# Optimization experiments

Hardware: AMD Instinct MI355X
Metric: run time of the kernel (lower is better)

## Reference

```python
import jax, jax.numpy as jnp
import numpy as np

B, T, NH, EX, VOCAB, NLAYER = 8, 510, 12, 768, 256, 6
NBLK = 2 * NLAYER - 1          # 11 blocks, all with out=ex
NE = T + 2                     # CustomEmb output dim = n_embd = 512
HD = EX // NH
EXIT_SCALE = 1.0 / float(np.sqrt(4 * NBLK))  # torch init divides 'exit' params by sqrt(#exit params)


def _ln(x, s, b):
    m = jnp.mean(x, axis=-1, keepdims=True)
    v = jnp.mean((x - m) ** 2, axis=-1, keepdims=True)
    return (x - m) * jax.lax.rsqrt(v + 1e-5) * s + b


def setup_inputs() -> dict:
    key = jax.random.key(0)
    ks = iter(jax.random.split(key, 40))
    def n(shape, scale=0.02):
        return jax.random.normal(next(ks), shape, jnp.float32) * scale
    inp = {}
    inp['idx'] = jax.random.randint(next(ks), (B, T), 0, 2)
    inp['lin_w'] = n((NE, EX)); inp['lin_b'] = n((EX,))
    # stacked per-block params (leading dim NBLK), torch Linear math y = x @ W + b with W stored (in,out)
    inp['ln1_s'] = jnp.ones((NBLK, EX), jnp.float32); inp['ln1_b'] = jnp.zeros((NBLK, EX), jnp.float32)
    inp['qw'] = n((NBLK, EX, EX)); inp['qb'] = n((NBLK, EX))
    inp['kw'] = n((NBLK, EX, EX)); inp['kb'] = n((NBLK, EX))
    inp['vw'] = n((NBLK, EX, EX)); inp['vb'] = n((NBLK, EX))
    inp['ew'] = n((NBLK, EX, EX)) * EXIT_SCALE; inp['eb'] = n((NBLK, EX)) * EXIT_SCALE
    inp['ln2_s'] = jnp.ones((NBLK, EX), jnp.float32); inp['ln2_b'] = jnp.zeros((NBLK, EX), jnp.float32)
    inp['m1w'] = n((NBLK, EX, 4 * EX)); inp['m1b'] = n((NBLK, 4 * EX))
    inp['m2w'] = n((NBLK, 4 * EX, EX)) * EXIT_SCALE; inp['m2b'] = n((NBLK, EX)) * EXIT_SCALE
    inp['lnf_s'] = jnp.ones((EX,), jnp.float32); inp['lnf_b'] = jnp.zeros((EX,), jnp.float32)
    inp['head_w'] = n((EX * T, VOCAB)); inp['head_b'] = n((VOCAB,))
    return inp


def reference(idx, lin_w, lin_b, ln1_s, ln1_b, qw, qb, kw, kb, vw, vb, ew, eb,
              ln2_s, ln2_b, m1w, m1b, m2w, m2b, lnf_s, lnf_b, head_w, head_b):
    # CustomEmb: one-hot of binary token + identity positional encoding -> [B,T,T+2]
    e0 = (idx == 0).astype(jnp.float32)
    e1 = (idx == 1).astype(jnp.float32)
    pos = jnp.broadcast_to(jnp.eye(T, dtype=jnp.float32), (B, T, T))
    x = jnp.concatenate([e0[:, :, None], e1[:, :, None], pos], axis=2)
    x = jax.nn.relu(x @ lin_w + lin_b)                       # [B,T,EX]
    mask = jnp.tril(jnp.ones((T, T), bool))
    inv_sqrt_d = 1.0 / float(np.sqrt(HD))

    def block(x, p):
        l1s, l1b, Qw, Qb, Kw, Kb, Vw, Vb, Ew, Eb, l2s, l2b, M1w, M1b, M2w, M2b = p
        h = _ln(x, l1s, l1b)
        q = (h @ Qw + Qb).reshape(B, T, NH, HD)
        k = (h @ Kw + Kb).reshape(B, T, NH, HD)
        v = (h @ Vw + Vb).reshape(B, T, NH, HD)
        att = jnp.einsum('bqhd,bkhd->bhqk', q, k) * inv_sqrt_d
        att = jnp.where(mask, att, -jnp.inf)
        probs = jax.nn.softmax(att, axis=-1)
        y = jnp.einsum('bhqk,bkhd->bqhd', probs, v).reshape(B, T, EX)
        x = x + y @ Ew + Eb
        h2 = _ln(x, l2s, l2b)
        x = x + jax.nn.relu(h2 @ M1w + M1b) @ M2w + M2b      # MLP depth=2: initial+relu+exit
        return x, None

    x, _ = jax.lax.scan(block, x, (ln1_s, ln1_b, qw, qb, kw, kb, vw, vb,
                                   ew, eb, ln2_s, ln2_b, m1w, m1b, m2w, m2b))
    x = _ln(x, lnf_s, lnf_b)
    return x.reshape(B, -1) @ head_w + head_b                # [B, VOCAB]
```

## Files before the change

kernel.cpp:

```cpp
#include <hip/hip_runtime.h>
#include <hip/hip_bf16.h>
#include <math.h>

constexpr int cB = 8, cT = 510, cNH = 12, cEX = 768, cVOC = 256, cNBLK = 11, cHD = 64;
constexpr int cMB = 512;
constexpr int cMP = 4096;
constexpr int cQKV = 3 * cEX;

typedef __attribute__((ext_vector_type(8))) short bf16x8;
typedef __attribute__((ext_vector_type(4))) float f32x4;
using bf16 = __hip_bfloat16;

__device__ inline void gload16(const void* g, void* l) {
    __builtin_amdgcn_global_load_lds((const __attribute__((address_space(1))) unsigned int*)g,
                                     (__attribute__((address_space(3))) unsigned int*)l, 16, 0, 0);
}
__device__ inline short f2bs(float f) {
    bf16 b = __float2bfloat16(f);
    return *reinterpret_cast<short*>(&b);
}

__global__ __launch_bounds__(256) void embed_kernel(
    const int* __restrict__ idx, const float* __restrict__ lin_w,
    const float* __restrict__ lin_b, float* __restrict__ x)
{
    int row = blockIdx.x;
    int b = row >> 9, t = row & 511;
    float* xr = x + (size_t)row * cEX;
    if (t >= cT) {
        for (int j = threadIdx.x; j < cEX; j += 256) xr[j] = 0.0f;
        return;
    }
    int tok = idx[b * cT + t] & 1;
    const float* wt = lin_w + (size_t)tok * cEX;
    const float* wp = lin_w + (size_t)(2 + t) * cEX;
    for (int j = threadIdx.x; j < cEX; j += 256) {
        float val = wt[j] + wp[j] + lin_b[j];
        xr[j] = fmaxf(val, 0.0f);
    }
}

template<typename OUT>
__global__ __launch_bounds__(256) void ln_wave(
    const float* __restrict__ in, const float* __restrict__ s,
    const float* __restrict__ bsh, OUT* __restrict__ out)
{
    const int wid = threadIdx.x >> 6, lane = threadIdx.x & 63;
    const int row = blockIdx.x * 4 + wid;
    const float* xr = in + (size_t)row * cEX;
    float4 v[3];
    float sum = 0.f, sq = 0.f;
#pragma unroll
    for (int p = 0; p < 3; ++p) {
        v[p] = *(const float4*)&xr[p * 256 + lane * 4];
        sum += v[p].x + v[p].y + v[p].z + v[p].w;
        sq  += v[p].x * v[p].x + v[p].y * v[p].y + v[p].z * v[p].z + v[p].w * v[p].w;
    }
#pragma unroll
    for (int off = 1; off < 64; off <<= 1) {
        sum += __shfl_xor(sum, off, 64);
        sq  += __shfl_xor(sq, off, 64);
    }
    float mean = sum * (1.0f / cEX);
    float var = sq * (1.0f / cEX) - mean * mean;
    float rstd = rsqrtf(var + 1e-5f);
    OUT* outr = out + (size_t)row * cEX;
#pragma unroll
    for (int p = 0; p < 3; ++p) {
        int c = p * 256 + lane * 4;
        float4 sv = *(const float4*)&s[c];
        float4 bv = *(const float4*)&bsh[c];
        float o0 = (v[p].x - mean) * rstd * sv.x + bv.x;
        float o1 = (v[p].y - mean) * rstd * sv.y + bv.y;
        float o2 = (v[p].z - mean) * rstd * sv.z + bv.z;
        float o3 = (v[p].w - mean) * rstd * sv.w + bv.w;
        if constexpr (sizeof(OUT) == 2) {
            short4 pk;
            pk.x = f2bs(o0); pk.y = f2bs(o1); pk.z = f2bs(o2); pk.w = f2bs(o3);
            *(short4*)&outr[c] = pk;
        } else {
            *(float4*)&outr[c] = make_float4(o0, o1, o2, o3);
        }
    }
}

__global__ __launch_bounds__(256) void transpose_w(
    const float* __restrict__ W, bf16* __restrict__ WT,
    int K, int N, size_t w_stride, size_t wt_stride, int wt_row_off)
{
    __shared__ float t[32][33];
    const float* Wb = W + (size_t)blockIdx.z * w_stride;
    bf16* WTb = WT + (size_t)blockIdx.z * wt_stride;
    int n0 = blockIdx.x * 32, k0 = blockIdx.y * 32;
    int c = threadIdx.x & 31, ty = threadIdx.x >> 5;
#pragma unroll
    for (int it = 0; it < 4; ++it) {
        int r = ty + it * 8;
        t[r][c] = Wb[(size_t)(k0 + r) * N + n0 + c];
    }
    __syncthreads();
#pragma unroll
    for (int it = 0; it < 4; ++it) {
        int a = ty + it * 8;
        WTb[(size_t)(wt_row_off + n0 + a) * K + k0 + c] = __float2bfloat16(t[c][a]);
    }
}

__global__ __launch_bounds__(256) void concat_bias(
    const float* __restrict__ qb, const float* __restrict__ kb,
    const float* __restrict__ vb, float* __restrict__ qkvb)
{
    int i = blockIdx.x * 256 + threadIdx.x;
    if (i >= cNBLK * cQKV) return;
    int blk = i / cQKV, c = i - blk * cQKV;
    const float* src; int cc = c;
    if (c < cEX)            { src = qb; }
    else if (c < 2 * cEX)   { src = kb; cc = c - cEX; }
    else                    { src = vb; cc = c - 2 * cEX; }
    qkvb[i] = src[(size_t)blk * cEX + cc];
}

template<int FM, int FN, bool RELU, bool RESID, bool OUTBF16, bool VT>
__global__ __launch_bounds__(256) void gemm_db(
    const short* __restrict__ A, const short* __restrict__ BT,
    const float* __restrict__ bias, const float* __restrict__ resid,
    void* __restrict__ Cout, short* __restrict__ vTr, int K, int N)
{
    constexpr int BM = FM * 32, BN = FN * 32;
    constexpr int TS = (BM + BN) * 64;
    constexpr int CA = BM / 32, CB = BN / 32;
    constexpr int LPT = CA + CB;
    __shared__ short lds[2 * TS];
    const int tid = threadIdx.x;
    const int lane = tid & 63, wid = tid >> 6;
    const int wm = wid >> 1, wn = wid & 1;
    const int bm = blockIdx.y * BM, bn = blockIdx.x * BN;
    const int li = lane & 15, gk = lane >> 4;

    f32x4 acc[FM][FN];
#pragma unroll
    for (int i = 0; i < FM; ++i)
#pragma unroll
        for (int j = 0; j < FN; ++j)
            acc[i][j] = f32x4{0.f, 0.f, 0.f, 0.f};

    auto stage = [&](int kt, int buf) {
        short* la = &lds[buf * TS];
        short* lb = la + BM * 64;
#pragma unroll
        for (int i = 0; i < CA; ++i) {
            int s = i * 256 + tid;
            int r = s >> 3, c = s & 7;
            gload16(A + (size_t)(bm + r) * K + kt * 64 + (c ^ (r & 7)) * 8,
                    (char*)la + (size_t)(i * 256 + wid * 64) * 16);
        }
#pragma unroll
        for (int i = 0; i < CB; ++i) {
            int s = i * 256 + tid;
            int r = s >> 3, c = s & 7;
            gload16(BT + (size_t)(bn + r) * K + kt * 64 + (c ^ (r & 7)) * 8,
                    (char*)lb + (size_t)(i * 256 + wid * 64) * 16);
        }
    };

    const int nkt = K >> 6;
    stage(0, 0);
    stage(1, 1);

    for (int t = 0; t < nkt; ++t) {
        if (t + 1 < nkt) {
            if constexpr (LPT == 8) asm volatile("s_waitcnt vmcnt(8)" ::: "memory");
            else                    asm volatile("s_waitcnt vmcnt(6)" ::: "memory");
        } else {
            asm volatile("s_waitcnt vmcnt(0)" ::: "memory");
        }
        __builtin_amdgcn_s_barrier();

        const short* la = &lds[(t & 1) * TS];
        const short* lb = la + BM * 64;
        bf16x8 af[FM][2], bf_[FN][2];
#pragma unroll
        for (int mi = 0; mi < FM; ++mi) {
            int row = wm * FM * 16 + mi * 16 + li;
#pragma unroll
            for (int ks = 0; ks < 2; ++ks)
                af[mi][ks] = *(const bf16x8*)&la[row * 64 + ((ks * 4 + gk) ^ (row & 7)) * 8];
        }
#pragma unroll
        for (int ni = 0; ni < FN; ++ni) {
            int row = wn * FN * 16 + ni * 16 + li;
#pragma unroll
            for (int ks = 0; ks < 2; ++ks)
                bf_[ni][ks] = *(const bf16x8*)&lb[row * 64 + ((ks * 4 + gk) ^ (row & 7)) * 8];
        }
        __builtin_amdgcn_s_setprio(1);
#pragma unroll
        for (int ks = 0; ks < 2; ++ks)
#pragma unroll
            for (int mi = 0; mi < FM; ++mi)
#pragma unroll
                for (int ni = 0; ni < FN; ++ni)
                    acc[mi][ni] = __builtin_amdgcn_mfma_f32_16x16x32_bf16(
                        af[mi][ks], bf_[ni][ks], acc[mi][ni], 0, 0, 0);
        __builtin_amdgcn_s_setprio(0);

        asm volatile("" ::: "memory");
        __builtin_amdgcn_s_barrier();
        if (t + 2 < nkt) stage(t + 2, t & 1);
    }

#pragma unroll
    for (int mi = 0; mi < FM; ++mi) {
#pragma unroll
        for (int ni = 0; ni < FN; ++ni) {
            int col = bn + wn * FN * 16 + ni * 16 + li;
            float bv = bias[col];
            int row0 = bm + wm * FM * 16 + mi * 16 + gk * 4;
            if (VT && col >= 2 * cEX) {
                short4 pk;
                pk.x = f2bs(acc[mi][ni][0] + bv);
                pk.y = f2bs(acc[mi][ni][1] + bv);
                pk.z = f2bs(acc[mi][ni][2] + bv);
                pk.w = f2bs(acc[mi][ni][3] + bv);
                *(short4*)&vTr[(size_t)(col - 2 * cEX) * cMP + row0] = pk;
            } else {
#pragma unroll
                for (int j = 0; j < 4; ++j) {
                    int row = row0 + j;
                    float v = acc[mi][ni][j] + bv;
                    if (RELU) v = fmaxf(v, 0.0f);
                    if (RESID) v += resid[(size_t)row * N + col];
                    if (OUTBF16)
                        ((bf16*)Cout)[(size_t)row * N + col] = __float2bfloat16(v);
                    else
                        ((float*)Cout)[(size_t)row * N + col] = v;
                }
            }
        }
    }
}

__global__ __launch_bounds__(256) void attn_mfma(
    const short* __restrict__ qkv, const short* __restrict__ vT, bf16* __restrict__ y)
{
    const int qt = blockIdx.x, h = blockIdx.y, b = blockIdx.z;
    __shared__ short Ks[32 * 64];
    __shared__ short Vs[64 * 32];
    __shared__ short Ss[4][16][40];
    const int tid = threadIdx.x;
    const int lane = tid & 63, wid = tid >> 6;
    const int li = lane & 15, gk = lane >> 4;

    const size_t rowb = (size_t)b * cMB;
    int qr = qt * 64 + wid * 16 + li;
    int qrc = qr < cT ? qr : cT - 1;
    const short* qrow = qkv + (rowb + qrc) * cQKV + h * cHD;
    bf16x8 qf0 = *(const bf16x8*)(qrow + gk * 8);
    bf16x8 qf1 = *(const bf16x8*)(qrow + 32 + gk * 8);

    f32x4 o[4];
    float mrow[4], lrow[4];
#pragma unroll
    for (int dt = 0; dt < 4; ++dt) o[dt] = f32x4{0.f, 0.f, 0.f, 0.f};
#pragma unroll
    for (int j = 0; j < 4; ++j) { mrow[j] = -3e38f; lrow[j] = 0.f; }

    const int kkey = tid >> 3, kclog = (tid & 7) ^ (kkey & 7);
    const int vd = tid >> 2,  vclog = (tid & 3) ^ (vd & 3);
    const int qloc = qt * 64 + wid * 16 + gk * 4;

    const int nkt = 2 * qt + 2;
    for (int kt = 0; kt < nkt; ++kt) {
        gload16(qkv + (rowb + kt * 32 + kkey) * cQKV + cEX + h * cHD + kclog * 8,
                (char*)Ks + wid * 1024);
        gload16(vT + (size_t)(h * cHD + vd) * cMP + rowb + kt * 32 + vclog * 8,
                (char*)Vs + wid * 1024);
        __syncthreads();

        f32x4 s0 = f32x4{0.f, 0.f, 0.f, 0.f}, s1 = f32x4{0.f, 0.f, 0.f, 0.f};
        {
            int key0 = li, key1 = 16 + li;
            bf16x8 k00 = *(const bf16x8*)&Ks[key0 * 64 + ((0 + gk) ^ (key0 & 7)) * 8];
            bf16x8 k01 = *(const bf16x8*)&Ks[key0 * 64 + ((4 + gk) ^ (key0 & 7)) * 8];
            bf16x8 k10 = *(const bf16x8*)&Ks[key1 * 64 + ((0 + gk) ^ (key1 & 7)) * 8];
            bf16x8 k11 = *(const bf16x8*)&Ks[key1 * 64 + ((4 + gk) ^ (key1 & 7)) * 8];
            s0 = __builtin_amdgcn_mfma_f32_16x16x32_bf16(qf0, k00, s0, 0, 0, 0);
            s0 = __builtin_amdgcn_mfma_f32_16x16x32_bf16(qf1, k01, s0, 0, 0, 0);
            s1 = __builtin_amdgcn_mfma_f32_16x16x32_bf16(qf0, k10, s1, 0, 0, 0);
            s1 = __builtin_amdgcn_mfma_f32_16x16x32_bf16(qf1, k11, s1, 0, 0, 0);
        }

        float sc0[4], sc1[4];
#pragma unroll
        for (int j = 0; j < 4; ++j) {
            int q = qloc + j;
            int key0 = kt * 32 + li, key1 = key0 + 16;
            sc0[j] = (key0 <= q) ? s0[j] * 0.125f : -3e38f;
            sc1[j] = (key1 <= q) ? s1[j] * 0.125f : -3e38f;
        }
        float p0[4], p1[4];
#pragma unroll
        for (int j = 0; j < 4; ++j) {
            float tm = fmaxf(sc0[j], sc1[j]);
            tm = fmaxf(tm, __shfl_xor(tm, 1, 16));
            tm = fmaxf(tm, __shfl_xor(tm, 2, 16));
            tm = fmaxf(tm, __shfl_xor(tm, 4, 16));
            tm = fmaxf(tm, __shfl_xor(tm, 8, 16));
            float mnew = fmaxf(mrow[j], tm);
            p0[j] = __expf(sc0[j] - mnew);
            p1[j] = __expf(sc1[j] - mnew);
            float ps = p0[j] + p1[j];
            ps += __shfl_xor(ps, 1, 16);
            ps += __shfl_xor(ps, 2, 16);
            ps += __shfl_xor(ps, 4, 16);
            ps += __shfl_xor(ps, 8, 16);
            float scale = __expf(mrow[j] - mnew);
            lrow[j] = lrow[j] * scale + ps;
            mrow[j] = mnew;
#pragma unroll
            for (int dt = 0; dt < 4; ++dt) o[dt][j] *= scale;
        }
#pragma unroll
        for (int j = 0; j < 4; ++j) {
            Ss[wid][gk * 4 + j][li]      = f2bs(p0[j]);
            Ss[wid][gk * 4 + j][16 + li] = f2bs(p1[j]);
        }
        bf16x8 pa = *(const bf16x8*)&Ss[wid][li][gk * 8];
#pragma unroll
        for (int dt = 0; dt < 4; ++dt) {
            int d = dt * 16 + li;
            bf16x8 vf = *(const bf16x8*)&Vs[d * 32 + (gk ^ (d & 3)) * 8];
            o[dt] = __builtin_amdgcn_mfma_f32_16x16x32_bf16(pa, vf, o[dt], 0, 0, 0);
        }
        __syncthreads();
    }

#pragma unroll
    for (int j = 0; j < 4; ++j) {
        int q = qloc + j;
        if (q >= cT) continue;
        float inv = 1.0f / lrow[j];
        bf16* yr = y + (rowb + q) * cEX + h * cHD;
#pragma unroll
        for (int dt = 0; dt < 4; ++dt)
            yr[dt * 16 + li] = __float2bfloat16(o[dt][j] * inv);
    }
}

__global__ __launch_bounds__(256) void head_part_kernel(
    const float* __restrict__ xf, const float* __restrict__ hw, float* __restrict__ part)
{
    __shared__ float xs[8][1536];
    const int tid = threadIdx.x;
    const int k0 = blockIdx.x * 1536;
    for (int i = tid; i < 8 * 1536; i += 256) {
        int bb = i / 1536, kk = i - bb * 1536;
        xs[bb][kk] = xf[(size_t)bb * (cMB * cEX) + k0 + kk];
    }
    __syncthreads();
    float acc[8] = {};
    const float* wp = hw + (size_t)k0 * cVOC + tid;
    for (int kk = 0; kk < 1536; ++kk) {
        float w = wp[(size_t)kk * cVOC];
#pragma unroll
        for (int bb = 0; bb < 8; ++bb) acc[bb] += xs[bb][kk] * w;
    }
#pragma unroll
    for (int bb = 0; bb < 8; ++bb)
        part[((size_t)blockIdx.x * 8 + bb) * cVOC + tid] = acc[bb];
}

__global__ __launch_bounds__(256) void head_reduce_kernel(
    const float* __restrict__ part, const float* __restrict__ hb, float* __restrict__ out)
{
    int i = blockIdx.x * 256 + threadIdx.x;
    int bb = i >> 8, vv = i & 255;
    float acc = hb[vv];
    for (int c = 0; c < 255; ++c) acc += part[((size_t)c * 8 + bb) * 256 + vv];
    out[i] = acc;
}

extern "C" void kernel_launch(void* const* d_in, const int* in_sizes, int n_in,
                              void* d_out, int out_size, void* d_ws, size_t ws_size,
                              hipStream_t stream) {
    (void)in_sizes; (void)n_in; (void)out_size; (void)ws_size;
    const int*   idx    = (const int*)d_in[0];
    const float* lin_w  = (const float*)d_in[1];
    const float* lin_b  = (const float*)d_in[2];
    const float* ln1_s  = (const float*)d_in[3];
    const float* ln1_b  = (const float*)d_in[4];
    const float* qw     = (const float*)d_in[5];
    const float* qbias  = (const float*)d_in[6];
    const float* kw     = (const float*)d_in[7];
    const float* kbias  = (const float*)d_in[8];
    const float* vw     = (const float*)d_in[9];
    const float* vbias  = (const float*)d_in[10];
    const float* ew     = (const float*)d_in[11];
    const float* ebias  = (const float*)d_in[12];
    const float* ln2_s  = (const float*)d_in[13];
    const float* ln2_b  = (const float*)d_in[14];
    const float* m1w    = (const float*)d_in[15];
    const float* m1b    = (const float*)d_in[16];
    const float* m2w    = (const float*)d_in[17];
    const float* m2b    = (const float*)d_in[18];
    const float* lnf_s  = (const float*)d_in[19];
    const float* lnf_b  = (const float*)d_in[20];
    const float* head_w = (const float*)d_in[21];
    const float* head_b = (const float*)d_in[22];
    float* out = (float*)d_out;

    const size_t act = (size_t)cMP * cEX;
    float* x    = (float*)d_ws;
    float* xf   = x + act;
    float* part = xf + act;
    float* qkvb = part + 255 * 8 * 256;
    short* qkv  = (short*)(qkvb + cNBLK * cQKV);
    short* vTr  = qkv + (size_t)cMP * cQKV;
    short* h    = vTr + (size_t)cEX * cMP;
    short* h2   = h + act;
    short* y    = h2 + act;
    short* u    = y + act;
    short* wqkvT = u + (size_t)cMP * 4 * cEX;
    short* weT   = wqkvT + (size_t)cNBLK * cQKV * cEX;
    short* wm1T  = weT + (size_t)cNBLK * cEX * cEX;
    short* wm2T  = wm1T + (size_t)cNBLK * cEX * 4 * cEX;

    transpose_w<<<dim3(24, 24, cNBLK), 256, 0, stream>>>(qw, (bf16*)wqkvT, cEX, cEX,
        (size_t)cEX * cEX, (size_t)cQKV * cEX, 0);
    transpose_w<<<dim3(24, 24, cNBLK), 256, 0, stream>>>(kw, (bf16*)wqkvT, cEX, cEX,
        (size_t)cEX * cEX, (size_t)cQKV * cEX, cEX);
    transpose_w<<<dim3(24, 24, cNBLK), 256, 0, stream>>>(vw, (bf16*)wqkvT, cEX, cEX,
        (size_t)cEX * cEX, (size_t)cQKV * cEX, 2 * cEX);
    transpose_w<<<dim3(24, 24, cNBLK), 256, 0, stream>>>(ew, (bf16*)weT, cEX, cEX,
        (size_t)cEX * cEX, (size_t)cEX * cEX, 0);
    transpose_w<<<dim3(96, 24, cNBLK), 256, 0, stream>>>(m1w, (bf16*)wm1T, cEX, 4 * cEX,
        (size_t)cEX * 4 * cEX, (size_t)cEX * 4 * cEX, 0);
    transpose_w<<<dim3(24, 96, cNBLK), 256, 0, stream>>>(m2w, (bf16*)wm2T, 4 * cEX, cEX,
        (size_t)cEX * 4 * cEX, (size_t)cEX * 4 * cEX, 0);
    concat_bias<<<(cNBLK * cQKV + 255) / 256, 256, 0, stream>>>(qbias, kbias, vbias, qkvb);

    embed_kernel<<<cMP, 256, 0, stream>>>(idx, lin_w, lin_b, x);

    for (int blk = 0; blk < cNBLK; ++blk) {
        size_t bo = (size_t)blk * cEX;
        ln_wave<bf16><<<cMP / 4, 256, 0, stream>>>(x, ln1_s + bo, ln1_b + bo, (bf16*)h);
        gemm_db<4, 4, false, false, true, true><<<dim3(cQKV / 128, cMP / 128), 256, 0, stream>>>(
            h, wqkvT + (size_t)blk * cQKV * cEX, qkvb + (size_t)blk * cQKV, nullptr,
            qkv, vTr, cEX, cQKV);
        attn_mfma<<<dim3(8, cNH, cB), 256, 0, stream>>>(qkv, vTr, (bf16*)y);
        gemm_db<2, 4, false, true, false, false><<<dim3(cEX / 128, cMP / 64), 256, 0, stream>>>(
            y, weT + (size_t)blk * cEX * cEX, ebias + bo, x, x, nullptr, cEX, cEX);
        ln_wave<bf16><<<cMP / 4, 256, 0, stream>>>(x, ln2_s + bo, ln2_b + bo, (bf16*)h2);
        gemm_db<4, 4, true, false, true, false><<<dim3(4 * cEX / 128, cMP / 128), 256, 0, stream>>>(
            h2, wm1T + (size_t)blk * cEX * 4 * cEX, m1b + (size_t)blk * 4 * cEX, nullptr,
            u, nullptr, cEX, 4 * cEX);
        gemm_db<2, 4, false, true, false, false><<<dim3(cEX / 128, cMP / 64), 256, 0, stream>>>(
            u, wm2T + (size_t)blk * cEX * 4 * cEX, m2b + bo, x, x, nullptr, 4 * cEX, cEX);
    }
    ln_wave<float><<<cMP / 4, 256, 0, stream>>>(x, lnf_s, lnf_b, xf);
    head_part_kernel<<<255, 256, 0, stream>>>(xf, head_w, part);
    head_reduce_kernel<<<8, 256, 0, stream>>>(part, head_b, out);
}
```

Baseline: 1.889 ms.

## Split GEMM k-step to overlap staging with MFMA; use 64-key attention tiles

In the GEMM main loop, the second half of each 64-wide K tile is now read from LDS before the barrier. The next stage's global-to-LDS load is then issued before the second batch of MFMAs, so the loads overlap with compute. In attention, each iteration now processes 64 keys instead of 32. This halves the number of loop trips, barriers and softmax reductions, at the cost of more LDS and registers and possibly lower occupancy. Causal masking is unchanged, but the diagonal tile now does a full 64-key block of wasted work.

```diff
diff --git a/kernel.cpp b/kernel.cpp
--- a/kernel.cpp
+++ b/kernel.cpp
@@ -178,35 +178,49 @@
 
         const short* la = &lds[(t & 1) * TS];
         const short* lb = la + BM * 64;
-        bf16x8 af[FM][2], bf_[FN][2];
+
+        bf16x8 af0[FM], bf0[FN];
 #pragma unroll
         for (int mi = 0; mi < FM; ++mi) {
             int row = wm * FM * 16 + mi * 16 + li;
-#pragma unroll
-            for (int ks = 0; ks < 2; ++ks)
-                af[mi][ks] = *(const bf16x8*)&la[row * 64 + ((ks * 4 + gk) ^ (row & 7)) * 8];
+            af0[mi] = *(const bf16x8*)&la[row * 64 + (gk ^ (row & 7)) * 8];
         }
 #pragma unroll
         for (int ni = 0; ni < FN; ++ni) {
             int row = wn * FN * 16 + ni * 16 + li;
-#pragma unroll
-            for (int ks = 0; ks < 2; ++ks)
-                bf_[ni][ks] = *(const bf16x8*)&lb[row * 64 + ((ks * 4 + gk) ^ (row & 7)) * 8];
+            bf0[ni] = *(const bf16x8*)&lb[row * 64 + (gk ^ (row & 7)) * 8];
         }
         __builtin_amdgcn_s_setprio(1);
 #pragma unroll
-        for (int ks = 0; ks < 2; ++ks)
-#pragma unroll
-            for (int mi = 0; mi < FM; ++mi)
-#pragma unroll
-                for (int ni = 0; ni < FN; ++ni)
-                    acc[mi][ni] = __builtin_amdgcn_mfma_f32_16x16x32_bf16(
-                        af[mi][ks], bf_[ni][ks], acc[mi][ni], 0, 0, 0);
+        for (int mi = 0; mi < FM; ++mi)
+#pragma unroll
+            for (int ni = 0; ni < FN; ++ni)
+                acc[mi][ni] = __builtin_amdgcn_mfma_f32_16x16x32_bf16(
+                    af0[mi], bf0[ni], acc[mi][ni], 0, 0, 0);
         __builtin_amdgcn_s_setprio(0);
 
-        asm volatile("" ::: "memory");
+        bf16x8 af1[FM], bf1[FN];
+#pragma unroll
+        for (int mi = 0; mi < FM; ++mi) {
+            int row = wm * FM * 16 + mi * 16 + li;
+            af1[mi] = *(const bf16x8*)&la[row * 64 + ((4 + gk) ^ (row & 7)) * 8];
+        }
+#pragma unroll
+        for (int ni = 0; ni < FN; ++ni) {
+            int row = wn * FN * 16 + ni * 16 + li;
+            bf1[ni] = *(const bf16x8*)&lb[row * 64 + ((4 + gk) ^ (row & 7)) * 8];
+        }
+        asm volatile("s_waitcnt lgkmcnt(0)" ::: "memory");
         __builtin_amdgcn_s_barrier();
         if (t + 2 < nkt) stage(t + 2, t & 1);
+        __builtin_amdgcn_s_setprio(1);
+#pragma unroll
+        for (int mi = 0; mi < FM; ++mi)
+#pragma unroll
+            for (int ni = 0; ni < FN; ++ni)
+                acc[mi][ni] = __builtin_amdgcn_mfma_f32_16x16x32_bf16(
+                    af1[mi], bf1[ni], acc[mi][ni], 0, 0, 0);
+        __builtin_amdgcn_s_setprio(0);
     }
 
 #pragma unroll
@@ -244,9 +258,9 @@
     const short* __restrict__ qkv, const short* __restrict__ vT, bf16* __restrict__ y)
 {
     const int qt = blockIdx.x, h = blockIdx.y, b = blockIdx.z;
-    __shared__ short Ks[32 * 64];
-    __shared__ short Vs[64 * 32];
-    __shared__ short Ss[4][16][40];
+    __shared__ short Ks[64 * 64];
+    __shared__ short Vs[64 * 64];
+    __shared__ short Ss[4][16][72];
     const int tid = threadIdx.x;
     const int lane = tid & 63, wid = tid >> 6;
     const int li = lane & 15, gk = lane >> 4;
@@ -265,51 +279,56 @@
 #pragma unroll
     for (int j = 0; j < 4; ++j) { mrow[j] = -3e38f; lrow[j] = 0.f; }
 
-    const int kkey = tid >> 3, kclog = (tid & 7) ^ (kkey & 7);
-    const int vd = tid >> 2,  vclog = (tid & 3) ^ (vd & 3);
     const int qloc = qt * 64 + wid * 16 + gk * 4;
 
-    const int nkt = 2 * qt + 2;
+    const int nkt = qt + 1;
     for (int kt = 0; kt < nkt; ++kt) {
-        gload16(qkv + (rowb + kt * 32 + kkey) * cQKV + cEX + h * cHD + kclog * 8,
-                (char*)Ks + wid * 1024);
-        gload16(vT + (size_t)(h * cHD + vd) * cMP + rowb + kt * 32 + vclog * 8,
-                (char*)Vs + wid * 1024);
+#pragma unroll
+        for (int i = 0; i < 2; ++i) {
+            int s = i * 256 + tid;
+            int r = s >> 3, c = s & 7;
+            gload16(qkv + (rowb + kt * 64 + r) * cQKV + cEX + h * cHD + (c ^ (r & 7)) * 8,
+                    (char*)Ks + (size_t)(i * 256 + wid * 64) * 16);
+        }
+#pragma unroll
+        for (int i = 0; i < 2; ++i) {
+            int s = i * 256 + tid;
+            int d = s >> 3, c = s & 7;
+            gload16(vT + (size_t)(h * cHD + d) * cMP + rowb + kt * 64 + (c ^ (d & 7)) * 8,
+                    (char*)Vs + (size_t)(i * 256 + wid * 64) * 16);
+        }
         __syncthreads();
 
-        f32x4 s0 = f32x4{0.f, 0.f, 0.f, 0.f}, s1 = f32x4{0.f, 0.f, 0.f, 0.f};
-        {
-            int key0 = li, key1 = 16 + li;
-            bf16x8 k00 = *(const bf16x8*)&Ks[key0 * 64 + ((0 + gk) ^ (key0 & 7)) * 8];
-            bf16x8 k01 = *(const bf16x8*)&Ks[key0 * 64 + ((4 + gk) ^ (key0 & 7)) * 8];
-            bf16x8 k10 = *(const bf16x8*)&Ks[key1 * 64 + ((0 + gk) ^ (key1 & 7)) * 8];
-            bf16x8 k11 = *(const bf16x8*)&Ks[key1 * 64 + ((4 + gk) ^ (key1 & 7)) * 8];
-            s0 = __builtin_amdgcn_mfma_f32_16x16x32_bf16(qf0, k00, s0, 0, 0, 0);
-            s0 = __builtin_amdgcn_mfma_f32_16x16x32_bf16(qf1, k01, s0, 0, 0, 0);
-            s1 = __builtin_amdgcn_mfma_f32_16x16x32_bf16(qf0, k10, s1, 0, 0, 0);
-            s1 = __builtin_amdgcn_mfma_f32_16x16x32_bf16(qf1, k11, s1, 0, 0, 0);
-        }
-
-        float sc0[4], sc1[4];
+        f32x4 sg[4];
+#pragma unroll
+        for (int g = 0; g < 4; ++g) sg[g] = f32x4{0.f, 0.f, 0.f, 0.f};
+#pragma unroll
+        for (int g = 0; g < 4; ++g) {
+            int key = g * 16 + li;
+            bf16x8 k0 = *(const bf16x8*)&Ks[key * 64 + (gk ^ (key & 7)) * 8];
+            bf16x8 k1 = *(const bf16x8*)&Ks[key * 64 + ((4 + gk) ^ (key & 7)) * 8];
+            sg[g] = __builtin_amdgcn_mfma_f32_16x16x32_bf16(qf0, k0, sg[g], 0, 0, 0);
+            sg[g] = __builtin_amdgcn_mfma_f32_16x16x32_bf16(qf1, k1, sg[g], 0, 0, 0);
+        }
+
 #pragma unroll
         for (int j = 0; j < 4; ++j) {
             int q = qloc + j;
-            int key0 = kt * 32 + li, key1 = key0 + 16;
-            sc0[j] = (key0 <= q) ? s0[j] * 0.125f : -3e38f;
-            sc1[j] = (key1 <= q) ? s1[j] * 0.125f : -3e38f;
-        }
-        float p0[4], p1[4];
-#pragma unroll
-        for (int j = 0; j < 4; ++j) {
-            float tm = fmaxf(sc0[j], sc1[j]);
+            float sc[4];
+#pragma unroll
+            for (int g = 0; g < 4; ++g) {
+                int kg = kt * 64 + g * 16 + li;
+                sc[g] = (kg <= q) ? sg[g][j] * 0.125f : -3e38f;
+            }
+            float tm = fmaxf(fmaxf(sc[0], sc[1]), fmaxf(sc[2], sc[3]));
             tm = fmaxf(tm, __shfl_xor(tm, 1, 16));
             tm = fmaxf(tm, __shfl_xor(tm, 2, 16));
             tm = fmaxf(tm, __shfl_xor(tm, 4, 16));
             tm = fmaxf(tm, __shfl_xor(tm, 8, 16));
             float mnew = fmaxf(mrow[j], tm);
-            p0[j] = __expf(sc0[j] - mnew);
-            p1[j] = __expf(sc1[j] - mnew);
-            float ps = p0[j] + p1[j];
+            float p[4], ps = 0.f;
+#pragma unroll
+            for (int g = 0; g < 4; ++g) { p[g] = __expf(sc[g] - mnew); ps += p[g]; }
             ps += __shfl_xor(ps, 1, 16);
             ps += __shfl_xor(ps, 2, 16);
             ps += __shfl_xor(ps, 4, 16);
@@ -319,18 +338,20 @@
             mrow[j] = mnew;
 #pragma unroll
             for (int dt = 0; dt < 4; ++dt) o[dt][j] *= scale;
-        }
-#pragma unroll
-        for (int j = 0; j < 4; ++j) {
-            Ss[wid][gk * 4 + j][li]      = f2bs(p0[j]);
-            Ss[wid][gk * 4 + j][16 + li] = f2bs(p1[j]);
-        }
-        bf16x8 pa = *(const bf16x8*)&Ss[wid][li][gk * 8];
+#pragma unroll
+            for (int g = 0; g < 4; ++g)
+                Ss[wid][gk * 4 + j][g * 16 + li] = f2bs(p[g]);
+        }
+
+        bf16x8 pa0 = *(const bf16x8*)&Ss[wid][li][gk * 8];
+        bf16x8 pa1 = *(const bf16x8*)&Ss[wid][li][32 + gk * 8];
 #pragma unroll
         for (int dt = 0; dt < 4; ++dt) {
             int d = dt * 16 + li;
-            bf16x8 vf = *(const bf16x8*)&Vs[d * 32 + (gk ^ (d & 3)) * 8];
-            o[dt] = __builtin_amdgcn_mfma_f32_16x16x32_bf16(pa, vf, o[dt], 0, 0, 0);
+            bf16x8 vf0 = *(const bf16x8*)&Vs[d * 64 + (gk ^ (d & 7)) * 8];
+            bf16x8 vf1 = *(const bf16x8*)&Vs[d * 64 + ((4 + gk) ^ (d & 7)) * 8];
+            o[dt] = __builtin_amdgcn_mfma_f32_16x16x32_bf16(pa0, vf0, o[dt], 0, 0, 0);
+            o[dt] = __builtin_amdgcn_mfma_f32_16x16x32_bf16(pa1, vf1, o[dt], 0, 0, 0);
         }
         __syncthreads();
     }
```

Result: faster. 1.794 ms (-5.0%).
